# Optimization experiments

Measured on AMD Instinct MI355X. Metric: run time of the kernel, lower is better.

The kernel has to match this reference:

```python
import jax, jax.numpy as jnp
import numpy as np

EPS = 1e-12  # matches torch F.normalize default eps


def setup_inputs() -> dict:
    key = jax.random.key(0)
    ks = jax.random.split(key, 8)
    B, N, D, H = 8, 2048, 128, 128
    s = 1.0 / np.sqrt(D)
    return {
        "x": jax.random.normal(ks[0], (B, N, D), dtype=jnp.float32),
        "edge_weight": jax.random.uniform(ks[1], (B, N, N), dtype=jnp.float32),
        "W0": jax.random.normal(ks[2], (D, H), dtype=jnp.float32) * s,
        "b0": jnp.zeros((H,), dtype=jnp.float32),
        "W1": jax.random.normal(ks[3], (H, H), dtype=jnp.float32) * s,
        "b1": jnp.zeros((H,), dtype=jnp.float32),
        "W2": jax.random.normal(ks[4], (H, H), dtype=jnp.float32) * s,
        "b2": jnp.zeros((H,), dtype=jnp.float32),
    }


def _adapt_conv(h, edge_weight, W, b, is_last):
    h = h @ W + b                                   # [B,N,H]
    norm = jnp.linalg.norm(h, axis=-1, keepdims=True)
    nh = h / jnp.maximum(norm, EPS)                 # L2 normalize (F.normalize)
    cos = jnp.einsum('bij,bkj->bik', nh, nh)        # [B,N,N] cosine similarity
    ew = edge_weight * cos                          # elementwise mask
    h = jnp.einsum('bpq,bqc->bpc', ew, h)           # weighted aggregation
    if not is_last:
        h = jax.nn.relu(h)                          # dropout p=0.0 -> identity
    return h


def reference(x, edge_weight, W0, b0, W1, b1, W2, b2):
    params = [(W0, b0), (W1, b1), (W2, b2)]
    h = x
    n_layers = len(params)
    for i, (W, b) in enumerate(params):
        h = _adapt_conv(h, edge_weight, W, b, is_last=(i == n_layers - 1))
    return h
```

## Files before the change

### kernel.cpp

```cpp
#include <hip/hip_runtime.h>
#include <hip/hip_bf16.h>
#include <math.h>


typedef __attribute__((ext_vector_type(8))) short bf16x8;
typedef __attribute__((ext_vector_type(4))) short bf16x4;
typedef __attribute__((ext_vector_type(4))) float f32x4;

static constexpr int kB = 8, kN = 2048, kH = 128;

static __device__ __forceinline__ ushort bf16bits(float f) {
    __hip_bfloat16 hb = __float2bfloat16(f);
    return *reinterpret_cast<ushort*>(&hb);
}

__global__ __launch_bounds__(256) void cvt_bf16_kernel(
    const float* __restrict__ src, ushort* __restrict__ dst, int n4)
{
    int i = blockIdx.x * 256 + threadIdx.x;
    if (i >= n4) return;
    float4 v = ((const float4*)src)[i];
    bf16x4 o;
    o[0] = (short)bf16bits(v.x); o[1] = (short)bf16bits(v.y);
    o[2] = (short)bf16bits(v.z); o[3] = (short)bf16bits(v.w);
    ((bf16x4*)dst)[i] = o;
}

__global__ __launch_bounds__(256) void cvt_wT_kernel(
    const float* __restrict__ W0, const float* __restrict__ W1,
    const float* __restrict__ W2, ushort* __restrict__ WT)
{
    const float* W = blockIdx.y == 0 ? W0 : (blockIdx.y == 1 ? W1 : W2);
    int i = blockIdx.x * 256 + threadIdx.x;
    int d = i >> 7, c = i & 127;
    WT[(size_t)blockIdx.y * kH * kH + c * kH + d] = bf16bits(W[d * kH + c]);
}

__global__ __launch_bounds__(256) void linear_tr_kernel(
    const ushort* __restrict__ h16, const ushort* __restrict__ WT,
    const float* __restrict__ bias, ushort* __restrict__ t16,
    ushort* __restrict__ tT16, float* __restrict__ invn)
{
    __shared__ float ssb[64][2];
    __shared__ ushort tr[128 * 72];

    const int tid = threadIdx.x, lane = tid & 63, wid = tid >> 6;
    const int wr = wid >> 1, wc = wid & 1, quad = lane >> 4, l16 = lane & 15;
    const int rowbase = blockIdx.x * 64;
    const int b = rowbase / kN, q0 = rowbase % kN;

    f32x4 acc[2][4];
#pragma unroll
    for (int i = 0; i < 2; ++i)
#pragma unroll
        for (int ct = 0; ct < 4; ++ct) acc[i][ct] = (f32x4){0.f, 0.f, 0.f, 0.f};

#pragma unroll
    for (int k = 0; k < 4; ++k) {
        bf16x8 Af[2], Bf[4];
#pragma unroll
        for (int i = 0; i < 2; ++i)
            Af[i] = *(const bf16x8*)&h16[(size_t)(rowbase + wr * 32 + i * 16 + l16) * kH + k * 32 + quad * 8];
#pragma unroll
        for (int ct = 0; ct < 4; ++ct)
            Bf[ct] = *(const bf16x8*)&WT[(size_t)(wc * 64 + ct * 16 + l16) * kH + k * 32 + quad * 8];
#pragma unroll
        for (int i = 0; i < 2; ++i)
#pragma unroll
            for (int ct = 0; ct < 4; ++ct)
                acc[i][ct] = __builtin_amdgcn_mfma_f32_16x16x32_bf16(Af[i], Bf[ct], acc[i][ct], 0, 0, 0);
    }

    float bsr[4];
#pragma unroll
    for (int ct = 0; ct < 4; ++ct) bsr[ct] = bias[wc * 64 + ct * 16 + l16];

    f32x4 ss[2] = {(f32x4){0,0,0,0}, (f32x4){0,0,0,0}};
#pragma unroll
    for (int i = 0; i < 2; ++i)
#pragma unroll
        for (int ct = 0; ct < 4; ++ct)
#pragma unroll
            for (int r = 0; r < 4; ++r) {
                float v = acc[i][ct][r] + bsr[ct];
                acc[i][ct][r] = v;
                ss[i][r] += v * v;
            }
#pragma unroll
    for (int step = 1; step < 16; step <<= 1)
#pragma unroll
        for (int i = 0; i < 2; ++i)
#pragma unroll
            for (int r = 0; r < 4; ++r) ss[i][r] += __shfl_xor(ss[i][r], step);

    if (l16 == 0)
#pragma unroll
        for (int i = 0; i < 2; ++i)
#pragma unroll
            for (int r = 0; r < 4; ++r)
                ssb[wr * 32 + i * 16 + quad * 4 + r][wc] = ss[i][r];
    __syncthreads();
    if (tid < 64) {
        float s2 = ssb[tid][0] + ssb[tid][1];
        invn[rowbase + tid] = 1.f / fmaxf(sqrtf(s2), 1e-12f);
    }

#pragma unroll
    for (int i = 0; i < 2; ++i)
#pragma unroll
        for (int ct = 0; ct < 4; ++ct)
#pragma unroll
            for (int r = 0; r < 4; ++r) {
                const int pl = wr * 32 + i * 16 + quad * 4 + r;
                const int c = wc * 64 + ct * 16 + l16;
                ushort bits = bf16bits(acc[i][ct][r]);
                t16[(size_t)(rowbase + pl) * kH + c] = bits;
                tr[c * 72 + pl] = bits;
            }
    __syncthreads();

    ushort* tTb = tT16 + (size_t)b * kH * kN;
#pragma unroll
    for (int it = 0; it < 4; ++it) {
        int idx = tid + 256 * it;
        int c = idx >> 3, ch = idx & 7;
        bf16x8 v = *(const bf16x8*)&tr[c * 72 + ch * 8];
        *(bf16x8*)&tTb[(size_t)c * kN + q0 + ch * 8] = v;
    }
}

__global__ __launch_bounds__(1024, 4) void agg_kernel(
    const ushort* __restrict__ t, const ushort* __restrict__ tT,
    const float* __restrict__ invn, const float* __restrict__ ew,
    ushort* __restrict__ hout, float* __restrict__ fout, int last)
{
    __shared__ ushort TQ[64 * 136];
    __shared__ ushort TT[128 * 72];
    __shared__ ushort Spm[64 * 72];
    __shared__ float invPs[64];

    const int b = blockIdx.y, pbase = blockIdx.x * 64;
    const int tid = threadIdx.x, lane = tid & 63, wid = tid >> 6;
    const int wp = wid >> 2, wq = wid & 3, quad = lane >> 4, l16 = lane & 15;

    const ushort* tb  = t  + (size_t)b * kN * kH;
    const ushort* tTb = tT + (size_t)b * kH * kN;
    const float*  ewb = ew + (size_t)b * kN * kN;
    const float*  invb = invn + b * kN;

    if (tid < 64) invPs[tid] = invb[pbase + tid];

    bf16x8 Af[4];
#pragma unroll
    for (int k = 0; k < 4; ++k)
        Af[k] = *(const bf16x8*)&tb[(size_t)(pbase + wp * 16 + l16) * kH + k * 32 + quad * 8];

    const int sqRow = tid >> 4, sqCh = tid & 15;
    const int stRow = tid >> 3, stCh = tid & 7;
    bf16x8 rQ = *(const bf16x8*)&tb[(size_t)sqRow * kH + sqCh * 8];
    bf16x8 rT = *(const bf16x8*)&tTb[(size_t)stRow * kN + stCh * 8];

    const int ewRow = pbase + wp * 16 + quad * 4;
    float ewc[4], invQc;
    {
        const int qc = wq * 16 + l16;
        invQc = invb[qc];
#pragma unroll
        for (int r = 0; r < 4; ++r) ewc[r] = ewb[(size_t)(ewRow + r) * kN + qc];
    }

    __syncthreads();
    float invPr[4];
#pragma unroll
    for (int r = 0; r < 4; ++r) invPr[r] = invPs[wp * 16 + quad * 4 + r];

    f32x4 oacc[2] = {(f32x4){0,0,0,0}, (f32x4){0,0,0,0}};

    for (int qt = 0; qt < kN / 64; ++qt) {
        *(bf16x8*)&TQ[sqRow * 136 + sqCh * 8] = rQ;
        *(bf16x8*)&TT[stRow * 72 + stCh * 8]  = rT;
        __syncthreads();

        float ewn[4] = {0.f, 0.f, 0.f, 0.f};
        float invQn = 0.f;
        if (qt + 1 < kN / 64) {
            const int qb2 = (qt + 1) * 64;
            rQ = *(const bf16x8*)&tb[(size_t)(qb2 + sqRow) * kH + sqCh * 8];
            rT = *(const bf16x8*)&tTb[(size_t)stRow * kN + qb2 + stCh * 8];
            const int qc = qb2 + wq * 16 + l16;
            invQn = invb[qc];
#pragma unroll
            for (int r = 0; r < 4; ++r) ewn[r] = ewb[(size_t)(ewRow + r) * kN + qc];
        }

        f32x4 dacc = (f32x4){0.f, 0.f, 0.f, 0.f};
#pragma unroll
        for (int k = 0; k < 4; ++k) {
            bf16x8 Bf = *(const bf16x8*)&TQ[(wq * 16 + l16) * 136 + k * 32 + quad * 8];
            dacc = __builtin_amdgcn_mfma_f32_16x16x32_bf16(Af[k], Bf, dacc, 0, 0, 0);
        }
#pragma unroll
        for (int r = 0; r < 4; ++r)
            Spm[(wp * 16 + quad * 4 + r) * 72 + wq * 16 + l16] = bf16bits(dacc[r] * ewc[r] * invQc);
        __syncthreads();

#pragma unroll
        for (int k = 0; k < 2; ++k) {
            bf16x8 Sa = *(const bf16x8*)&Spm[(wp * 16 + l16) * 72 + k * 32 + quad * 8];
#pragma unroll
            for (int ct = 0; ct < 2; ++ct) {
                bf16x8 Bb = *(const bf16x8*)&TT[(wq * 32 + ct * 16 + l16) * 72 + k * 32 + quad * 8];
                oacc[ct] = __builtin_amdgcn_mfma_f32_16x16x32_bf16(Sa, Bb, oacc[ct], 0, 0, 0);
            }
        }
        __syncthreads();

#pragma unroll
        for (int r = 0; r < 4; ++r) ewc[r] = ewn[r];
        invQc = invQn;
    }

#pragma unroll
    for (int ct = 0; ct < 2; ++ct)
#pragma unroll
        for (int r = 0; r < 4; ++r) {
            const int p = pbase + wp * 16 + quad * 4 + r;
            const int c = wq * 32 + ct * 16 + l16;
            float v = oacc[ct][r] * invPr[r];
            if (!last) {
                hout[(size_t)b * kN * kH + (size_t)p * kH + c] = bf16bits(fmaxf(v, 0.f));
            } else {
                fout[(size_t)b * kN * kH + (size_t)p * kH + c] = v;
            }
        }
}

extern "C" void kernel_launch(void* const* d_in, const int* in_sizes, int n_in,
                              void* d_out, int out_size, void* d_ws, size_t ws_size,
                              hipStream_t stream) {
    const float* x  = (const float*)d_in[0];
    const float* ew = (const float*)d_in[1];
    const float* W0 = (const float*)d_in[2];
    const float* b0 = (const float*)d_in[3];
    const float* W1 = (const float*)d_in[4];
    const float* b1 = (const float*)d_in[5];
    const float* W2 = (const float*)d_in[6];
    const float* b2 = (const float*)d_in[7];
    const float* bias[3] = {b0, b1, b2};

    const size_t nBNH = (size_t)kB * kN * kH;
    ushort* h16  = (ushort*)d_ws;
    ushort* t16  = h16 + nBNH;
    ushort* tT16 = t16 + nBNH;
    float*  invn = (float*)(tT16 + nBNH);
    ushort* WT   = (ushort*)(invn + (size_t)kB * kN);
    float*  out  = (float*)d_out;

    cvt_bf16_kernel<<<(int)(nBNH / 4 + 255) / 256, 256, 0, stream>>>(x, h16, (int)(nBNH / 4));
    cvt_wT_kernel<<<dim3(64, 3), 256, 0, stream>>>(W0, W1, W2, WT);

    for (int layer = 0; layer < 3; ++layer) {
        linear_tr_kernel<<<kB * kN / 64, 256, 0, stream>>>(
            h16, WT + (size_t)layer * kH * kH, bias[layer], t16, tT16, invn);
        agg_kernel<<<dim3(kN / 64, kB), 1024, 0, stream>>>(
            t16, tT16, invn, ew, h16, out, layer == 2 ? 1 : 0);
    }
}
```

Before: 341.1 us.

## Restructure aggregation kernel with 32x32 MFMA, split-K over waves, register-resident fragments

```diff
diff --git a/kernel.cpp b/kernel.cpp
--- a/kernel.cpp
+++ b/kernel.cpp
@@ -3,15 +3,19 @@
 #include <math.h>
 
 
-typedef __attribute__((ext_vector_type(8))) short bf16x8;
-typedef __attribute__((ext_vector_type(4))) short bf16x4;
-typedef __attribute__((ext_vector_type(4))) float f32x4;
+typedef __attribute__((ext_vector_type(8)))  short bf16x8;
+typedef __attribute__((ext_vector_type(4)))  short bf16x4;
+typedef __attribute__((ext_vector_type(4)))  float f32x4;
+typedef __attribute__((ext_vector_type(16))) float f32x16;
 
 static constexpr int kB = 8, kN = 2048, kH = 128;
 
 static __device__ __forceinline__ ushort bf16bits(float f) {
     __hip_bfloat16 hb = __float2bfloat16(f);
     return *reinterpret_cast<ushort*>(&hb);
+}
+static __device__ __forceinline__ unsigned pk2(float lo, float hi) {
+    return (unsigned)bf16bits(lo) | ((unsigned)bf16bits(hi) << 16);
 }
 
 __global__ __launch_bounds__(256) void cvt_bf16_kernel(
@@ -129,110 +133,163 @@
     }
 }
 
-__global__ __launch_bounds__(1024, 4) void agg_kernel(
+__global__ __launch_bounds__(512, 2) void agg_kernel(
     const ushort* __restrict__ t, const ushort* __restrict__ tT,
     const float* __restrict__ invn, const float* __restrict__ ew,
     ushort* __restrict__ hout, float* __restrict__ fout, int last)
 {
-    __shared__ ushort TQ[64 * 136];
-    __shared__ ushort TT[128 * 72];
-    __shared__ ushort Spm[64 * 72];
-    __shared__ float invPs[64];
-
-    const int b = blockIdx.y, pbase = blockIdx.x * 64;
+    __shared__ char lds[65536];
+
+    const int b = blockIdx.x, pbase = blockIdx.y * 64;
     const int tid = threadIdx.x, lane = tid & 63, wid = tid >> 6;
-    const int wp = wid >> 2, wq = wid & 3, quad = lane >> 4, l16 = lane & 15;
+    const int wp = wid >> 2, wq = wid & 3;
+    const int l31 = lane & 31, h = lane >> 5;
 
     const ushort* tb  = t  + (size_t)b * kN * kH;
     const ushort* tTb = tT + (size_t)b * kH * kN;
     const float*  ewb = ew + (size_t)b * kN * kN;
     const float*  invb = invn + b * kN;
 
-    if (tid < 64) invPs[tid] = invb[pbase + tid];
-
-    bf16x8 Af[4];
-#pragma unroll
-    for (int k = 0; k < 4; ++k)
-        Af[k] = *(const bf16x8*)&tb[(size_t)(pbase + wp * 16 + l16) * kH + k * 32 + quad * 8];
-
-    const int sqRow = tid >> 4, sqCh = tid & 15;
-    const int stRow = tid >> 3, stCh = tid & 7;
-    bf16x8 rQ = *(const bf16x8*)&tb[(size_t)sqRow * kH + sqCh * 8];
-    bf16x8 rT = *(const bf16x8*)&tTb[(size_t)stRow * kN + stCh * 8];
-
-    const int ewRow = pbase + wp * 16 + quad * 4;
-    float ewc[4], invQc;
+    char* myEw = lds + wid * 8192;
+    const int pbg = pbase + wp * 32;
+
+    bf16x8 tP[8];
+#pragma unroll
+    for (int m = 0; m < 8; ++m)
+        tP[m] = *(const bf16x8*)&tb[(size_t)(pbg + l31) * kH + m * 16 + h * 8];
+
+    f32x16 oacc[4];
+#pragma unroll
+    for (int ct = 0; ct < 4; ++ct)
+#pragma unroll
+        for (int r = 0; r < 16; ++r) oacc[ct][r] = 0.f;
+
+    const int sQ = (lane & 15) * 4;
+    const int sR = lane >> 4;
+
+    f32x4 eC[8]; f32x4 iqC;
     {
-        const int qc = wq * 16 + l16;
-        invQc = invb[qc];
-#pragma unroll
-        for (int r = 0; r < 4; ++r) ewc[r] = ewb[(size_t)(ewRow + r) * kN + qc];
+        const int qb = wq * 64;
+        iqC = *(const f32x4*)&invb[qb + sQ];
+#pragma unroll
+        for (int j = 0; j < 8; ++j)
+            eC[j] = *(const f32x4*)&ewb[(size_t)(pbg + 4 * j + sR) * kN + qb + sQ];
+    }
+
+    auto buildFrags = [&](const f32x16 s, int st, bf16x8* out2) {
+        f32x4 ef[4];
+#pragma unroll
+        for (int g = 0; g < 4; ++g)
+            ef[g] = *(const f32x4*)&myEw[l31 * 256 +
+                     ((128 * st + 32 * g + 16 * h) ^ ((l31 & 15) << 4))];
+        float sv[16];
+#pragma unroll
+        for (int r = 0; r < 16; ++r) sv[r] = s[r] * ef[r >> 2][r & 3];
+#pragma unroll
+        for (int kk = 0; kk < 2; ++kk) {
+            const int e0 = kk * 8;
+            unsigned a0 = pk2(sv[e0 + 0], sv[e0 + 1]);
+            unsigned a1 = pk2(sv[e0 + 2], sv[e0 + 3]);
+            unsigned b0 = pk2(sv[e0 + 4], sv[e0 + 5]);
+            unsigned b1 = pk2(sv[e0 + 6], sv[e0 + 7]);
+            const unsigned ta0 = (unsigned)__shfl_xor((int)a0, 32);
+            const unsigned ta1 = (unsigned)__shfl_xor((int)a1, 32);
+            const unsigned tb0 = (unsigned)__shfl_xor((int)b0, 32);
+            const unsigned tb1 = (unsigned)__shfl_xor((int)b1, 32);
+            union { unsigned u[4]; bf16x8 v; } U;
+            U.u[0] = h ? tb0 : a0;
+            U.u[1] = h ? tb1 : a1;
+            U.u[2] = h ? b0  : ta0;
+            U.u[3] = h ? b1  : ta1;
+            out2[kk] = U.v;
+        }
+    };
+
+    for (int i = 0; i < 8; ++i) {
+        const int qb = (4 * i + wq) * 64;
+
+#pragma unroll
+        for (int j = 0; j < 8; ++j) {
+            const int row = 4 * j + sR;
+            f32x4 e = eC[j] * iqC;
+            *(f32x4*)&myEw[row * 256 + ((sQ * 4) ^ ((row & 15) << 4))] = e;
+        }
+
+        f32x16 s0, s1;
+#pragma unroll
+        for (int r = 0; r < 16; ++r) { s0[r] = 0.f; s1[r] = 0.f; }
+#pragma unroll
+        for (int m = 0; m < 8; ++m) {
+            bf16x8 a0 = *(const bf16x8*)&tb[(size_t)(qb + l31) * kH + m * 16 + h * 8];
+            bf16x8 a1 = *(const bf16x8*)&tb[(size_t)(qb + 32 + l31) * kH + m * 16 + h * 8];
+            s0 = __builtin_amdgcn_mfma_f32_32x32x16_bf16(a0, tP[m], s0, 0, 0, 0);
+            s1 = __builtin_amdgcn_mfma_f32_32x32x16_bf16(a1, tP[m], s1, 0, 0, 0);
+        }
+
+        bf16x8 aw[4];
+        buildFrags(s0, 0, &aw[0]);
+        buildFrags(s1, 1, &aw[2]);
+
+        if (i < 7) {
+            const int qb2 = (4 * (i + 1) + wq) * 64;
+            iqC = *(const f32x4*)&invb[qb2 + sQ];
+#pragma unroll
+            for (int j = 0; j < 8; ++j)
+                eC[j] = *(const f32x4*)&ewb[(size_t)(pbg + 4 * j + sR) * kN + qb2 + sQ];
+        }
+
+#pragma unroll
+        for (int kkt = 0; kkt < 4; ++kkt) {
+#pragma unroll
+            for (int ct = 0; ct < 4; ++ct) {
+                bf16x8 Bf = *(const bf16x8*)&tTb[(size_t)(32 * ct + l31) * kN + qb + 16 * kkt + 8 * h];
+                oacc[ct] = __builtin_amdgcn_mfma_f32_32x32x16_bf16(aw[kkt], Bf, oacc[ct], 0, 0, 0);
+            }
+        }
     }
 
     __syncthreads();
-    float invPr[4];
-#pragma unroll
-    for (int r = 0; r < 4; ++r) invPr[r] = invPs[wp * 16 + quad * 4 + r];
-
-    f32x4 oacc[2] = {(f32x4){0,0,0,0}, (f32x4){0,0,0,0}};
-
-    for (int qt = 0; qt < kN / 64; ++qt) {
-        *(bf16x8*)&TQ[sqRow * 136 + sqCh * 8] = rQ;
-        *(bf16x8*)&TT[stRow * 72 + stCh * 8]  = rT;
+    float* OL = (float*)lds;
+#pragma unroll
+    for (int w = 0; w < 4; ++w) {
+        if (wq == w) {
+#pragma unroll
+            for (int ct = 0; ct < 4; ++ct)
+#pragma unroll
+                for (int r = 0; r < 16; ++r) {
+                    const int pl = wp * 32 + (r & 3) + 8 * (r >> 2) + 4 * h;
+                    const int idx = pl * 128 + 32 * ct + l31;
+                    if (w == 0) OL[idx] = oacc[ct][r];
+                    else        OL[idx] += oacc[ct][r];
+                }
+        }
         __syncthreads();
-
-        float ewn[4] = {0.f, 0.f, 0.f, 0.f};
-        float invQn = 0.f;
-        if (qt + 1 < kN / 64) {
-            const int qb2 = (qt + 1) * 64;
-            rQ = *(const bf16x8*)&tb[(size_t)(qb2 + sqRow) * kH + sqCh * 8];
-            rT = *(const bf16x8*)&tTb[(size_t)stRow * kN + qb2 + stCh * 8];
-            const int qc = qb2 + wq * 16 + l16;
-            invQn = invb[qc];
-#pragma unroll
-            for (int r = 0; r < 4; ++r) ewn[r] = ewb[(size_t)(ewRow + r) * kN + qc];
-        }
-
-        f32x4 dacc = (f32x4){0.f, 0.f, 0.f, 0.f};
-#pragma unroll
-        for (int k = 0; k < 4; ++k) {
-            bf16x8 Bf = *(const bf16x8*)&TQ[(wq * 16 + l16) * 136 + k * 32 + quad * 8];
-            dacc = __builtin_amdgcn_mfma_f32_16x16x32_bf16(Af[k], Bf, dacc, 0, 0, 0);
-        }
-#pragma unroll
-        for (int r = 0; r < 4; ++r)
-            Spm[(wp * 16 + quad * 4 + r) * 72 + wq * 16 + l16] = bf16bits(dacc[r] * ewc[r] * invQc);
-        __syncthreads();
-
-#pragma unroll
-        for (int k = 0; k < 2; ++k) {
-            bf16x8 Sa = *(const bf16x8*)&Spm[(wp * 16 + l16) * 72 + k * 32 + quad * 8];
-#pragma unroll
-            for (int ct = 0; ct < 2; ++ct) {
-                bf16x8 Bb = *(const bf16x8*)&TT[(wq * 32 + ct * 16 + l16) * 72 + k * 32 + quad * 8];
-                oacc[ct] = __builtin_amdgcn_mfma_f32_16x16x32_bf16(Sa, Bb, oacc[ct], 0, 0, 0);
-            }
-        }
-        __syncthreads();
-
-#pragma unroll
-        for (int r = 0; r < 4; ++r) ewc[r] = ewn[r];
-        invQc = invQn;
-    }
-
-#pragma unroll
-    for (int ct = 0; ct < 2; ++ct)
-#pragma unroll
-        for (int r = 0; r < 4; ++r) {
-            const int p = pbase + wp * 16 + quad * 4 + r;
-            const int c = wq * 32 + ct * 16 + l16;
-            float v = oacc[ct][r] * invPr[r];
-            if (!last) {
-                hout[(size_t)b * kN * kH + (size_t)p * kH + c] = bf16bits(fmaxf(v, 0.f));
-            } else {
-                fout[(size_t)b * kN * kH + (size_t)p * kH + c] = v;
-            }
-        }
+    }
+
+    {
+        const int p = tid >> 3, cb = (tid & 7) * 16;
+        const float ip = invb[pbase + p];
+        const size_t gbase = (size_t)b * kN * kH + (size_t)(pbase + p) * kH + cb;
+        if (!last) {
+#pragma unroll
+            for (int u = 0; u < 2; ++u) {
+                bf16x8 o;
+#pragma unroll
+                for (int k = 0; k < 8; ++k)
+                    o[k] = (short)bf16bits(fmaxf(OL[p * 128 + cb + u * 8 + k] * ip, 0.f));
+                *(bf16x8*)&hout[gbase + u * 8] = o;
+            }
+        } else {
+#pragma unroll
+            for (int u = 0; u < 4; ++u) {
+                f32x4 o;
+#pragma unroll
+                for (int k = 0; k < 4; ++k)
+                    o[k] = OL[p * 128 + cb + u * 4 + k] * ip;
+                *(f32x4*)&fout[gbase + u * 4] = o;
+            }
+        }
+    }
 }
 
 extern "C" void kernel_launch(void* const* d_in, const int* in_sizes, int n_in,
@@ -262,7 +319,7 @@
     for (int layer = 0; layer < 3; ++layer) {
         linear_tr_kernel<<<kB * kN / 64, 256, 0, stream>>>(
             h16, WT + (size_t)layer * kH * kH, bias[layer], t16, tT16, invn);
-        agg_kernel<<<dim3(kN / 64, kB), 1024, 0, stream>>>(
+        agg_kernel<<<dim3(kB, kN / 64), 512, 0, stream>>>(
             t16, tT16, invn, ew, h16, out, layer == 2 ? 1 : 0);
     }
 }
```

After: 452.8 us. 32.8% more time.
